# Kernel tuning notes

Measured on AMD Instinct MI355X. Metric: run time of the kernel, lower is better.

The kernel has to match this reference:

```python
import jax, jax.numpy as jnp
import numpy as np

B, S, D, H = 2, 2048, 2048, 16
HD = D // H
DFF = 4 * D
EPS = 1e-5


def _gelu(x):
    # tanh-approximate GELU as in the torch module
    c = jnp.sqrt(jnp.asarray(2.0 / jnp.pi, dtype=x.dtype))
    return 0.5 * x * (1.0 + jnp.tanh(c * (x + 0.044715 * x ** 3)))


def _layernorm(x, scale, shift):
    mean = jnp.mean(x, axis=-1, keepdims=True)
    var = jnp.mean((x - mean) ** 2, axis=-1, keepdims=True)  # unbiased=False
    return scale * (x - mean) / jnp.sqrt(var + EPS) + shift


def setup_inputs() -> dict:
    key = jax.random.key(0)
    ks = jax.random.split(key, 8)
    std = 0.02
    return {
        "x": jax.random.normal(ks[0], (B, S, D), dtype=jnp.float32),
        "Wq": std * jax.random.normal(ks[1], (D, D), dtype=jnp.float32),
        "Wk": std * jax.random.normal(ks[2], (D, D), dtype=jnp.float32),
        "Wv": std * jax.random.normal(ks[3], (D, D), dtype=jnp.float32),
        "Wo": std * jax.random.normal(ks[4], (D, D), dtype=jnp.float32),
        "bo": jnp.zeros((D,), dtype=jnp.float32),
        "ln1_scale": jnp.ones((D,), dtype=jnp.float32),
        "ln1_shift": jnp.zeros((D,), dtype=jnp.float32),
        "ln2_scale": jnp.ones((D,), dtype=jnp.float32),
        "ln2_shift": jnp.zeros((D,), dtype=jnp.float32),
        "W1": std * jax.random.normal(ks[5], (D, DFF), dtype=jnp.float32),
        "b1": jnp.zeros((DFF,), dtype=jnp.float32),
        "W2": std * jax.random.normal(ks[6], (DFF, D), dtype=jnp.float32),
        "b2": jnp.zeros((D,), dtype=jnp.float32),
    }


def _attention(x, Wq, Wk, Wv, Wo, bo):
    b, s, d = x.shape
    q = (x @ Wq).reshape(b, s, H, HD).transpose(0, 2, 1, 3)  # bhsd
    k = (x @ Wk).reshape(b, s, H, HD).transpose(0, 2, 1, 3)
    v = (x @ Wv).reshape(b, s, H, HD).transpose(0, 2, 1, 3)
    scores = jnp.einsum("bhqd,bhkd->bhqk", q, k)
    causal = jnp.tril(jnp.ones((s, s), dtype=bool))
    scores = jnp.where(causal, scores, -jnp.inf)
    w = jax.nn.softmax(scores / jnp.sqrt(jnp.asarray(HD, dtype=x.dtype)), axis=-1)
    ctx = jnp.einsum("bhqk,bhkd->bhqd", w, v)
    ctx = ctx.transpose(0, 2, 1, 3).reshape(b, s, d)
    return ctx @ Wo + bo


def reference(x, Wq, Wk, Wv, Wo, bo, ln1_scale, ln1_shift, ln2_scale, ln2_shift, W1, b1, W2, b2):
    # pre-LN transformer block; dropout rate 0 -> identity
    h = x + _attention(_layernorm(x, ln1_scale, ln1_shift), Wq, Wk, Wv, Wo, bo)
    y = _gelu(_layernorm(h, ln2_scale, ln2_shift) @ W1 + b1)
    return h + (y @ W2 + b2)
```

## Files before the change

kernel.cpp:

```cpp
#include <hip/hip_runtime.h>
#include <cmath>


typedef unsigned short u16;
typedef unsigned int   u32;
typedef float  f32x4  __attribute__((ext_vector_type(4)));
typedef short  s16x8  __attribute__((ext_vector_type(8)));
typedef short  s16x4  __attribute__((ext_vector_type(4)));
typedef __bf16 bf16x8 __attribute__((ext_vector_type(8)));

#define DEV __device__ __forceinline__

DEV u16 f2bf(float f) {
  union { float f; u32 u; } v; v.f = f;
  u32 u = v.u;
  u += 0x7fffu + ((u >> 16) & 1u);
  return (u16)(u >> 16);
}

DEV f32x4 mfma16(s16x8 a, s16x8 b, f32x4 c) {
  return __builtin_amdgcn_mfma_f32_16x16x32_bf16(
      __builtin_bit_cast(bf16x8, a), __builtin_bit_cast(bf16x8, b), c, 0, 0, 0);
}

DEV float gelu_f(float x) {
  const float c = 0.7978845608028654f;
  const float z = c * (x + 0.044715f * x * x * x);
  const float e = __expf(2.0f * z);
  const float th = 1.0f - 2.0f / (e + 1.0f);
  return 0.5f * x * (1.0f + th);
}

DEV void gload16(const u16* g, u16* l) {
  __builtin_amdgcn_global_load_lds(
      (const __attribute__((address_space(1))) u32*)(const void*)g,
      (__attribute__((address_space(3))) u32*)(void*)l, 16, 0, 0);
}

__global__ __launch_bounds__(256) void transpose_cast(
    const float* __restrict__ W, u16* __restrict__ Wt, int K, int N) {
  __shared__ float tile[32][33];
  const int n0 = blockIdx.x * 32, k0 = blockIdx.y * 32;
  const int tx = threadIdx.x, ty = threadIdx.y;
#pragma unroll
  for (int i = 0; i < 4; ++i)
    tile[ty + 8 * i][tx] = W[(size_t)(k0 + ty + 8 * i) * N + n0 + tx];
  __syncthreads();
#pragma unroll
  for (int i = 0; i < 4; ++i)
    Wt[(size_t)(n0 + ty + 8 * i) * K + k0 + tx] = f2bf(tile[tx][ty + 8 * i]);
}

__global__ __launch_bounds__(256) void transpose_v(
    const u16* __restrict__ QKV, u16* __restrict__ VT) {
  __shared__ u16 tile[32][33];
  const int s0 = blockIdx.x * 32;
  const int d0 = blockIdx.y * 32;
  const int bh = blockIdx.z;
  const int b = bh >> 4, h = bh & 15;
  const int tx = threadIdx.x, ty = threadIdx.y;
  const u16* src = QKV + (long)b * 2048 * 6144 + 4096 + h * 128;
#pragma unroll
  for (int i = 0; i < 4; ++i)
    tile[ty + 8 * i][tx] = src[(long)(s0 + ty + 8 * i) * 6144 + d0 + tx];
  __syncthreads();
  u16* dst = VT + (long)bh * 128 * 2048;
#pragma unroll
  for (int i = 0; i < 4; ++i)
    dst[(long)(d0 + ty + 8 * i) * 2048 + s0 + tx] = tile[tx][ty + 8 * i];
}

__global__ __launch_bounds__(256) void ln_kernel(
    const float* __restrict__ X, const float* __restrict__ sc,
    const float* __restrict__ sh, u16* __restrict__ Y) {
  const int row = blockIdx.x, t = threadIdx.x;
  const float* xr = X + (size_t)row * 2048;
  float4 v0 = ((const float4*)xr)[t];
  float4 v1 = ((const float4*)xr)[t + 256];
  float s  = v0.x + v0.y + v0.z + v0.w + v1.x + v1.y + v1.z + v1.w;
  float qs = v0.x*v0.x + v0.y*v0.y + v0.z*v0.z + v0.w*v0.w
           + v1.x*v1.x + v1.y*v1.y + v1.z*v1.z + v1.w*v1.w;
#pragma unroll
  for (int off = 1; off < 64; off <<= 1) {
    s  += __shfl_xor(s, off);
    qs += __shfl_xor(qs, off);
  }
  __shared__ float rs[4], rq[4];
  if ((t & 63) == 0) { rs[t >> 6] = s; rq[t >> 6] = qs; }
  __syncthreads();
  const float st = rs[0] + rs[1] + rs[2] + rs[3];
  const float qt = rq[0] + rq[1] + rq[2] + rq[3];
  const float mean = st * (1.0f / 2048.0f);
  const float var  = qt * (1.0f / 2048.0f) - mean * mean;
  const float rstd = rsqrtf(var + 1e-5f);

  u16* yr = Y + (size_t)row * 2048;
  const int c0 = t * 4, c1 = 1024 + t * 4;
  s16x4 o0, o1;
  o0[0] = (short)f2bf(sc[c0+0] * (v0.x - mean) * rstd + sh[c0+0]);
  o0[1] = (short)f2bf(sc[c0+1] * (v0.y - mean) * rstd + sh[c0+1]);
  o0[2] = (short)f2bf(sc[c0+2] * (v0.z - mean) * rstd + sh[c0+2]);
  o0[3] = (short)f2bf(sc[c0+3] * (v0.w - mean) * rstd + sh[c0+3]);
  o1[0] = (short)f2bf(sc[c1+0] * (v1.x - mean) * rstd + sh[c1+0]);
  o1[1] = (short)f2bf(sc[c1+1] * (v1.y - mean) * rstd + sh[c1+1]);
  o1[2] = (short)f2bf(sc[c1+2] * (v1.z - mean) * rstd + sh[c1+2]);
  o1[3] = (short)f2bf(sc[c1+3] * (v1.w - mean) * rstd + sh[c1+3]);
  *(s16x4*)(yr + c0) = o0;
  *(s16x4*)(yr + c1) = o1;
}

template<int MHALF, int STORE_BF16, int BIAS, int RES, int GELU_ACT>
__global__ __launch_bounds__(512, 2) void gemm8(
    const u16* __restrict__ A, const u16* __restrict__ Bt,
    const float* __restrict__ bias, const float* __restrict__ res,
    float* __restrict__ Cf, u16* __restrict__ Cb,
    int M, int N, int K, int rr, int rc) {
  constexpr int NPH   = 2 * MHALF;
  constexpr int ABUFS = (MHALF == 2) ? 2 : 3;
  constexpr int ASZ   = 8192 * MHALF;
  constexpr int BOFF  = ABUFS * ASZ;
  __shared__ u16 lds[BOFF + 2 * 16384];

  const int t9 = threadIdx.x;
  const int l = t9 & 63, w = t9 >> 6;
  const int r16 = l & 15, quad = l >> 4;
  const int wm = w >> 2, wn = w & 3;

  const int nbx = N >> 8;
  const int bid = blockIdx.x;
  const int xcd = bid & 7, j = bid >> 3;
  const int nregc = nbx / rc;
  const int m_t = (xcd / nregc) * rr + (j % rr);
  const int n_t = (xcd % nregc) * rc + (j / rr);
  const long m0 = (long)m_t * (128 * MHALF);
  const long n0 = (long)n_t * 256;

  const int NT = K >> 6;
  const int srow = t9 >> 3;
  const int scol = (t9 & 7) ^ (srow & 7);

  const u16* Abase = A  + (m0 + srow) * (long)K + scol * 8;
  const u16* Bbase = Bt + (n0 + srow) * (long)K + scol * 8;
  const long rowK64  = 64 * (long)K;
  const long rowK128 = 128 * (long)K;

  #define STAGE_A(tile, h) { \
    u16* d = &lds[((tile) % ABUFS) * ASZ + (h) * 8192 + w * 512]; \
    const u16* s = Abase + (h) * rowK128 + (long)(tile) * 64; \
    gload16(s, d); gload16(s + rowK64, d + 4096); }
  #define STAGE_B(tile, h) { \
    u16* d = &lds[BOFF + ((tile) & 1) * 16384 + (h) * 8192 + w * 512]; \
    const u16* s = Bbase + (h) * rowK128 + (long)(tile) * 64; \
    gload16(s, d); gload16(s + rowK64, d + 4096); }

  f32x4 acc[4 * MHALF][4] = {};

  if (MHALF == 2) {
    STAGE_B(0, 0); STAGE_B(0, 1); STAGE_A(0, 0); STAGE_A(0, 1);
    STAGE_B(1, 0); STAGE_B(1, 1);
    asm volatile("s_waitcnt vmcnt(4)" ::: "memory");
  } else {
    STAGE_B(0, 0); STAGE_B(0, 1); STAGE_A(0, 0); STAGE_A(1, 0);
    STAGE_B(1, 0); STAGE_B(1, 1);
    asm volatile("s_waitcnt vmcnt(6)" ::: "memory");
  }
  __builtin_amdgcn_sched_barrier(0);
  __builtin_amdgcn_s_barrier();

  s16x8 bf_[4][2];
  for (int t = 0; t < NT; ++t) {
    const int ab = t % ABUFS;
    const u16* Abuf = &lds[ab * ASZ];
    const u16* Bbuf = &lds[BOFF + (t & 1) * 16384];
#pragma unroll
    for (int p = 0; p < NPH; ++p) {
      if (p == 0) {
#pragma unroll
        for (int ni = 0; ni < 4; ++ni) {
          const int brow = wn * 64 + ni * 16 + r16;
#pragma unroll
          for (int ks = 0; ks < 2; ++ks)
            bf_[ni][ks] = *(const s16x8*)&Bbuf[brow * 64 + ((ks * 4 + quad) ^ (brow & 7)) * 8];
        }
      }
      s16x8 af[2][2];
#pragma unroll
      for (int mi = 0; mi < 2; ++mi) {
        const int arow = (MHALF == 2 ? wm * 128 : wm * 64) + (2 * p + mi) * 16 + r16;
#pragma unroll
        for (int ks = 0; ks < 2; ++ks)
          af[mi][ks] = *(const s16x8*)&Abuf[arow * 64 + ((ks * 4 + quad) ^ (arow & 7)) * 8];
      }
      if (MHALF == 2) {
        if (p < 2)       { if (t + 1 < NT) STAGE_A(t + 1, p); }
        else             { if (t + 2 < NT) STAGE_B(t + 2, p - 2); }
      } else {
        if (p == 0)      { if (t + 2 < NT) STAGE_A(t + 2, 0); }
        else             { if (t + 2 < NT) { STAGE_B(t + 2, 0); STAGE_B(t + 2, 1); } }
      }
      __builtin_amdgcn_sched_barrier(0);
      __builtin_amdgcn_s_barrier();
      asm volatile("s_waitcnt lgkmcnt(0)" ::: "memory");
      __builtin_amdgcn_sched_barrier(0);
      __builtin_amdgcn_s_setprio(1);
#pragma unroll
      for (int mi = 0; mi < 2; ++mi)
#pragma unroll
        for (int ni = 0; ni < 4; ++ni)
#pragma unroll
          for (int ks = 0; ks < 2; ++ks)
            acc[2 * p + mi][ni] = mfma16(af[mi][ks], bf_[ni][ks], acc[2 * p + mi][ni]);
      __builtin_amdgcn_s_setprio(0);
      __builtin_amdgcn_sched_barrier(0);
      if (p == NPH - 1) {
        if (MHALF == 2) {
          if (t + 2 < NT) { asm volatile("s_waitcnt vmcnt(4)" ::: "memory"); }
          else            { asm volatile("s_waitcnt vmcnt(0)" ::: "memory"); }
        } else {
          if (t + 2 < NT) { asm volatile("s_waitcnt vmcnt(6)" ::: "memory"); }
          else            { asm volatile("s_waitcnt vmcnt(0)" ::: "memory"); }
        }
        __builtin_amdgcn_sched_barrier(0);
      }
      __builtin_amdgcn_s_barrier();
    }
  }
  #undef STAGE_A
  #undef STAGE_B

#pragma unroll
  for (int mi = 0; mi < 4 * MHALF; ++mi) {
#pragma unroll
    for (int ni = 0; ni < 4; ++ni) {
#pragma unroll
      for (int r = 0; r < 4; ++r) {
        const long gr = m0 + (MHALF == 2 ? wm * 128 : wm * 64) + mi * 16 + quad * 4 + r;
        const long gc = n0 + wn * 64 + ni * 16 + r16;
        float v = acc[mi][ni][r];
        if (BIAS)     v += bias[gc];
        if (GELU_ACT) v  = gelu_f(v);
        if (RES)      v += res[gr * N + gc];
        if (STORE_BF16) Cb[gr * N + gc] = f2bf(v);
        else            Cf[gr * N + gc] = v;
      }
    }
  }
}

__global__ __launch_bounds__(256) void attn_kernel(
    const u16* __restrict__ QKV, const u16* __restrict__ VT,
    u16* __restrict__ CTX) {
  __shared__ u16 Ks[2][64 * 128];
  __shared__ u16 Vs[2][128 * 64];
  __shared__ u16 Pl[4][16 * 64];

  const int t = threadIdx.x;
  const int lane = t & 63, w = t >> 6;
  const int r16 = lane & 15, quad = lane >> 4;
  const int h = blockIdx.y, b = blockIdx.z;
  const long LDQ = 6144;
  const u16* Qb = QKV + (long)b * 2048 * LDQ + h * 128;
  const u16* Kb = Qb + 2048;
  const u16* Vtb = VT + (long)(b * 16 + h) * 128 * 2048;
  u16* Pw = Pl[w];
  const float scale = 0.08838834764831845f;

  const int k_row = t >> 4;
  const int k_slot = t & 15;
  const int v_row = t >> 3;
  const int v_slot = t & 7;

#define STAGE_KV(kt_, buf_)                                                    \
  {                                                                            \
    const int kb_ = (kt_) * 64;                                                \
    _Pragma("unroll") for (int i = 0; i < 4; ++i) {                            \
      const int row = i * 16 + k_row;                                          \
      gload16(Kb + (long)(kb_ + row) * LDQ + (k_slot ^ (row & 7)) * 8,         \
              &Ks[buf_][i * 2048 + w * 512]);                                  \
    }                                                                          \
    _Pragma("unroll") for (int i = 0; i < 4; ++i) {                            \
      const int d_ = i * 32 + v_row;                                           \
      gload16(Vtb + (long)d_ * 2048 + kb_ + (v_slot ^ (d_ & 7)) * 8,           \
              &Vs[buf_][i * 2048 + w * 512]);                                  \
    }                                                                          \
  }

  for (int half = 0; half < 2; ++half) {
    const int qt = half ? (31 - (int)blockIdx.x) : (int)blockIdx.x;
    const int qw = qt * 64 + w * 16;

    s16x8 aq[4];
#pragma unroll
    for (int ks = 0; ks < 4; ++ks)
      aq[ks] = *(const s16x8*)(Qb + (long)(qw + r16) * LDQ + ks * 32 + quad * 8);

    f32x4 o[8] = {};
    float mrun[4], lrun[4];
#pragma unroll
    for (int r = 0; r < 4; ++r) { mrun[r] = -1e30f; lrun[r] = 0.0f; }

    __builtin_amdgcn_s_barrier();
    STAGE_KV(0, 0);
    asm volatile("s_waitcnt vmcnt(0)" ::: "memory");
    __builtin_amdgcn_s_barrier();

    for (int kt = 0; kt <= qt; ++kt) {
      const int kbase = kt * 64;
      const int cur = kt & 1;
      if (kt < qt) STAGE_KV(kt + 1, cur ^ 1);

      if (kbase <= qw + 15) {
        f32x4 sc[4];
#pragma unroll
        for (int kh = 0; kh < 4; ++kh) {
          f32x4 z = {};
          sc[kh] = z;
          const int krow = kh * 16 + r16;
#pragma unroll
          for (int ks = 0; ks < 4; ++ks) {
            const s16x8 bk =
                *(const s16x8*)&Ks[cur][krow * 128 + ((ks * 4 + quad) ^ (krow & 7)) * 8];
            sc[kh] = mfma16(aq[ks], bk, sc[kh]);
          }
        }
        const bool need_mask = (kbase + 63 > qw);
        float alpha[4];
#pragma unroll
        for (int r = 0; r < 4; ++r) {
          const int q = qw + quad * 4 + r;
          float sv[4];
#pragma unroll
          for (int kh = 0; kh < 4; ++kh) {
            float s = sc[kh][r] * scale;
            if (need_mask && (kbase + kh * 16 + r16 > q)) s = -1e30f;
            sv[kh] = s;
          }
          float mx = fmaxf(fmaxf(sv[0], sv[1]), fmaxf(sv[2], sv[3]));
#pragma unroll
          for (int off = 1; off < 16; off <<= 1) mx = fmaxf(mx, __shfl_xor(mx, off));
          const float mn = fmaxf(mrun[r], mx);
          alpha[r] = __expf(mrun[r] - mn);
          mrun[r] = mn;
          const int prow = quad * 4 + r;
          float ps = 0.0f;
#pragma unroll
          for (int kh = 0; kh < 4; ++kh) {
            const float p = __expf(sv[kh] - mn);
            ps += p;
            Pw[(prow * 64 + kh * 16 + r16) ^ ((prow & 7) << 3)] = f2bf(p);
          }
          lrun[r] = lrun[r] * alpha[r] + ps;
        }
        if (alpha[0] != 1.0f || alpha[1] != 1.0f || alpha[2] != 1.0f || alpha[3] != 1.0f) {
#pragma unroll
          for (int ds = 0; ds < 8; ++ds)
#pragma unroll
            for (int r = 0; r < 4; ++r) o[ds][r] *= alpha[r];
        }
#pragma unroll
        for (int s = 0; s < 2; ++s) {
          const s16x8 ap =
              *(const s16x8*)&Pw[(r16 * 64 + s * 32 + quad * 8) ^ ((r16 & 7) << 3)];
#pragma unroll
          for (int ds = 0; ds < 8; ++ds) {
            const int d = ds * 16 + r16;
            const s16x8 bv =
                *(const s16x8*)&Vs[cur][d * 64 + ((s * 4 + quad) ^ (d & 7)) * 8];
            o[ds] = mfma16(ap, bv, o[ds]);
          }
        }
      }

      asm volatile("s_waitcnt vmcnt(0)" ::: "memory");
      __builtin_amdgcn_s_barrier();
    }

#pragma unroll
    for (int r = 0; r < 4; ++r)
#pragma unroll
      for (int off = 1; off < 16; off <<= 1) lrun[r] += __shfl_xor(lrun[r], off);

#pragma unroll
    for (int ds = 0; ds < 8; ++ds)
#pragma unroll
      for (int r = 0; r < 4; ++r) {
        const float v = o[ds][r] / lrun[r];
        CTX[(long)(b * 2048 + qw + quad * 4 + r) * 2048 + h * 128 + ds * 16 + r16] = f2bf(v);
      }
  }
#undef STAGE_KV
}

extern "C" void kernel_launch(void* const* d_in, const int* in_sizes, int n_in,
                              void* d_out, int out_size, void* d_ws, size_t ws_size,
                              hipStream_t stream) {
  (void)in_sizes; (void)n_in; (void)out_size; (void)ws_size;
  const float* x    = (const float*)d_in[0];
  const float* Wq   = (const float*)d_in[1];
  const float* Wk   = (const float*)d_in[2];
  const float* Wv   = (const float*)d_in[3];
  const float* Wo   = (const float*)d_in[4];
  const float* bo   = (const float*)d_in[5];
  const float* ln1s = (const float*)d_in[6];
  const float* ln1b = (const float*)d_in[7];
  const float* ln2s = (const float*)d_in[8];
  const float* ln2b = (const float*)d_in[9];
  const float* W1   = (const float*)d_in[10];
  const float* b1   = (const float*)d_in[11];
  const float* W2   = (const float*)d_in[12];
  const float* b2   = (const float*)d_in[13];
  float* out = (float*)d_out;

  const int Mtok = 4096, D = 2048, DFF = 8192, NQKV = 6144;

  char* w = (char*)d_ws;
  u16* Wt_qkv = (u16*)w;  w += (size_t)NQKV * D * 2;
  u16* Wt_o   = (u16*)w;  w += (size_t)D * D * 2;
  u16* Wt_1   = (u16*)w;  w += (size_t)DFF * D * 2;
  u16* Wt_2   = (u16*)w;  w += (size_t)D * DFF * 2;
  u16* Xln    = (u16*)w;  w += (size_t)Mtok * D * 2;
  u16* QKV    = (u16*)w;  w += (size_t)Mtok * NQKV * 2;
  u16* CTX    = (u16*)w;  w += (size_t)Mtok * D * 2;
  u16* Y1     = QKV;
  u16* VTb    = Wt_qkv;
  float* Hbuf = (float*)w; w += (size_t)Mtok * D * 4;

  const dim3 tb(32, 8, 1);
  transpose_cast<<<dim3(D / 32, D / 32), tb, 0, stream>>>(Wq, Wt_qkv,                    D, D);
  transpose_cast<<<dim3(D / 32, D / 32), tb, 0, stream>>>(Wk, Wt_qkv + (size_t)D * D,    D, D);
  transpose_cast<<<dim3(D / 32, D / 32), tb, 0, stream>>>(Wv, Wt_qkv + (size_t)2 * D * D,D, D);
  transpose_cast<<<dim3(D / 32, D / 32), tb, 0, stream>>>(Wo, Wt_o,                      D, D);
  transpose_cast<<<dim3(DFF / 32, D / 32), tb, 0, stream>>>(W1, Wt_1,                    D, DFF);
  transpose_cast<<<dim3(D / 32, DFF / 32), tb, 0, stream>>>(W2, Wt_2,                    DFF, D);

  ln_kernel<<<Mtok, 256, 0, stream>>>(x, ln1s, ln1b, Xln);

  gemm8<1, 1, 0, 0, 0><<<dim3(768), 512, 0, stream>>>(
      Xln, Wt_qkv, nullptr, nullptr, nullptr, QKV, Mtok, NQKV, D, 16, 6);

  transpose_v<<<dim3(64, 4, 32), tb, 0, stream>>>(QKV, VTb);

  attn_kernel<<<dim3(16, 16, 2), 256, 0, stream>>>(QKV, VTb, CTX);

  gemm8<1, 0, 1, 1, 0><<<dim3(256), 512, 0, stream>>>(
      CTX, Wt_o, bo, x, Hbuf, nullptr, Mtok, D, D, 8, 4);

  ln_kernel<<<Mtok, 256, 0, stream>>>(Hbuf, ln2s, ln2b, Xln);

  gemm8<2, 1, 1, 0, 1><<<dim3(512), 512, 0, stream>>>(
      Xln, Wt_1, b1, nullptr, nullptr, Y1, Mtok, DFF, D, 8, 8);

  gemm8<1, 0, 1, 1, 0><<<dim3(256), 512, 0, stream>>>(
      Y1, Wt_2, b2, Hbuf, out, nullptr, Mtok, D, DFF, 8, 4);
}
```

Before: 624.9 us.

## Add 256x256-tile GEMM kernel with split-K for FFN down-projection

Adds a dedicated gemm256 kernel with 256x256 output tiles and double-buffered A/B staging (four-phase schedule), used for the FFN up-projection. The down-projection now runs split-K over two K halves with a 256x256 tile (256 blocks), writing partial sums into a scratch buffer aliased onto the W1 weight workspace, followed by a separate reduce kernel that adds bias and residual. gemm8 is simplified to the 128-row path only. This is meant to raise data reuse and occupancy for the large GEMMs, at the cost of extra fp32 partial-sum traffic and an extra kernel launch.

```diff
diff --git a/kernel.cpp b/kernel.cpp
--- a/kernel.cpp
+++ b/kernel.cpp
@@ -4,10 +4,10 @@
 
 typedef unsigned short u16;
 typedef unsigned int   u32;
-typedef float  f32x4  __attribute__((ext_vector_type(4)));
-typedef short  s16x8  __attribute__((ext_vector_type(8)));
-typedef short  s16x4  __attribute__((ext_vector_type(4)));
-typedef __bf16 bf16x8 __attribute__((ext_vector_type(8)));
+typedef float  f32x4   __attribute__((ext_vector_type(4)));
+typedef short  s16x8   __attribute__((ext_vector_type(8)));
+typedef short  s16x4   __attribute__((ext_vector_type(4)));
+typedef __bf16 bf16x8  __attribute__((ext_vector_type(8)));
 
 #define DEV __device__ __forceinline__
 
@@ -109,15 +109,14 @@
   *(s16x4*)(yr + c1) = o1;
 }
 
-template<int MHALF, int STORE_BF16, int BIAS, int RES, int GELU_ACT>
+template<int STORE_BF16, int BIAS, int RES, int GELU_ACT>
 __global__ __launch_bounds__(512, 2) void gemm8(
     const u16* __restrict__ A, const u16* __restrict__ Bt,
     const float* __restrict__ bias, const float* __restrict__ res,
     float* __restrict__ Cf, u16* __restrict__ Cb,
     int M, int N, int K, int rr, int rc) {
-  constexpr int NPH   = 2 * MHALF;
-  constexpr int ABUFS = (MHALF == 2) ? 2 : 3;
-  constexpr int ASZ   = 8192 * MHALF;
+  constexpr int ABUFS = 3;
+  constexpr int ASZ   = 8192;
   constexpr int BOFF  = ABUFS * ASZ;
   __shared__ u16 lds[BOFF + 2 * 16384];
 
@@ -132,7 +131,7 @@
   const int nregc = nbx / rc;
   const int m_t = (xcd / nregc) * rr + (j % rr);
   const int n_t = (xcd % nregc) * rc + (j / rr);
-  const long m0 = (long)m_t * (128 * MHALF);
+  const long m0 = (long)m_t * 128;
   const long n0 = (long)n_t * 256;
 
   const int NT = K >> 6;
@@ -144,36 +143,29 @@
   const long rowK64  = 64 * (long)K;
   const long rowK128 = 128 * (long)K;
 
-  #define STAGE_A(tile, h) { \
+  #define STAGE_A8(tile, h) { \
     u16* d = &lds[((tile) % ABUFS) * ASZ + (h) * 8192 + w * 512]; \
     const u16* s = Abase + (h) * rowK128 + (long)(tile) * 64; \
     gload16(s, d); gload16(s + rowK64, d + 4096); }
-  #define STAGE_B(tile, h) { \
+  #define STAGE_B8(tile, h) { \
     u16* d = &lds[BOFF + ((tile) & 1) * 16384 + (h) * 8192 + w * 512]; \
     const u16* s = Bbase + (h) * rowK128 + (long)(tile) * 64; \
     gload16(s, d); gload16(s + rowK64, d + 4096); }
 
-  f32x4 acc[4 * MHALF][4] = {};
-
-  if (MHALF == 2) {
-    STAGE_B(0, 0); STAGE_B(0, 1); STAGE_A(0, 0); STAGE_A(0, 1);
-    STAGE_B(1, 0); STAGE_B(1, 1);
-    asm volatile("s_waitcnt vmcnt(4)" ::: "memory");
-  } else {
-    STAGE_B(0, 0); STAGE_B(0, 1); STAGE_A(0, 0); STAGE_A(1, 0);
-    STAGE_B(1, 0); STAGE_B(1, 1);
-    asm volatile("s_waitcnt vmcnt(6)" ::: "memory");
-  }
+  f32x4 acc[4][4] = {};
+
+  STAGE_B8(0, 0); STAGE_B8(0, 1); STAGE_A8(0, 0); STAGE_A8(1, 0);
+  STAGE_B8(1, 0); STAGE_B8(1, 1);
+  asm volatile("s_waitcnt vmcnt(6)" ::: "memory");
   __builtin_amdgcn_sched_barrier(0);
   __builtin_amdgcn_s_barrier();
 
   s16x8 bf_[4][2];
   for (int t = 0; t < NT; ++t) {
-    const int ab = t % ABUFS;
-    const u16* Abuf = &lds[ab * ASZ];
+    const u16* Abuf = &lds[(t % ABUFS) * ASZ];
     const u16* Bbuf = &lds[BOFF + (t & 1) * 16384];
 #pragma unroll
-    for (int p = 0; p < NPH; ++p) {
+    for (int p = 0; p < 2; ++p) {
       if (p == 0) {
 #pragma unroll
         for (int ni = 0; ni < 4; ++ni) {
@@ -186,18 +178,13 @@
       s16x8 af[2][2];
 #pragma unroll
       for (int mi = 0; mi < 2; ++mi) {
-        const int arow = (MHALF == 2 ? wm * 128 : wm * 64) + (2 * p + mi) * 16 + r16;
+        const int arow = wm * 64 + (2 * p + mi) * 16 + r16;
 #pragma unroll
         for (int ks = 0; ks < 2; ++ks)
           af[mi][ks] = *(const s16x8*)&Abuf[arow * 64 + ((ks * 4 + quad) ^ (arow & 7)) * 8];
       }
-      if (MHALF == 2) {
-        if (p < 2)       { if (t + 1 < NT) STAGE_A(t + 1, p); }
-        else             { if (t + 2 < NT) STAGE_B(t + 2, p - 2); }
-      } else {
-        if (p == 0)      { if (t + 2 < NT) STAGE_A(t + 2, 0); }
-        else             { if (t + 2 < NT) { STAGE_B(t + 2, 0); STAGE_B(t + 2, 1); } }
-      }
+      if (p == 0) { if (t + 2 < NT) STAGE_A8(t + 2, 0); }
+      else        { if (t + 2 < NT) { STAGE_B8(t + 2, 0); STAGE_B8(t + 2, 1); } }
       __builtin_amdgcn_sched_barrier(0);
       __builtin_amdgcn_s_barrier();
       asm volatile("s_waitcnt lgkmcnt(0)" ::: "memory");
@@ -212,29 +199,24 @@
             acc[2 * p + mi][ni] = mfma16(af[mi][ks], bf_[ni][ks], acc[2 * p + mi][ni]);
       __builtin_amdgcn_s_setprio(0);
       __builtin_amdgcn_sched_barrier(0);
-      if (p == NPH - 1) {
-        if (MHALF == 2) {
-          if (t + 2 < NT) { asm volatile("s_waitcnt vmcnt(4)" ::: "memory"); }
-          else            { asm volatile("s_waitcnt vmcnt(0)" ::: "memory"); }
-        } else {
-          if (t + 2 < NT) { asm volatile("s_waitcnt vmcnt(6)" ::: "memory"); }
-          else            { asm volatile("s_waitcnt vmcnt(0)" ::: "memory"); }
-        }
+      if (p == 1) {
+        if (t + 2 < NT) { asm volatile("s_waitcnt vmcnt(6)" ::: "memory"); }
+        else            { asm volatile("s_waitcnt vmcnt(0)" ::: "memory"); }
         __builtin_amdgcn_sched_barrier(0);
       }
       __builtin_amdgcn_s_barrier();
     }
   }
-  #undef STAGE_A
-  #undef STAGE_B
-
-#pragma unroll
-  for (int mi = 0; mi < 4 * MHALF; ++mi) {
+  #undef STAGE_A8
+  #undef STAGE_B8
+
+#pragma unroll
+  for (int mi = 0; mi < 4; ++mi) {
 #pragma unroll
     for (int ni = 0; ni < 4; ++ni) {
 #pragma unroll
       for (int r = 0; r < 4; ++r) {
-        const long gr = m0 + (MHALF == 2 ? wm * 128 : wm * 64) + mi * 16 + quad * 4 + r;
+        const long gr = m0 + wm * 64 + mi * 16 + quad * 4 + r;
         const long gc = n0 + wn * 64 + ni * 16 + r16;
         float v = acc[mi][ni][r];
         if (BIAS)     v += bias[gc];
@@ -244,6 +226,153 @@
         else            Cf[gr * N + gc] = v;
       }
     }
+  }
+}
+
+template<int STORE_BF16, int BIAS, int RES, int GELU_ACT, int SPLITK>
+__global__ __launch_bounds__(512, 2) void gemm256(
+    const u16* __restrict__ A, const u16* __restrict__ Bt,
+    const float* __restrict__ bias, const float* __restrict__ res,
+    float* __restrict__ Cf, u16* __restrict__ Cb, float* __restrict__ Cf2,
+    int M, int N, int K, int rr, int rc) {
+  __shared__ u16 ldsA[2 * 16384];
+  __shared__ u16 ldsB[2 * 16384];
+
+  const int t9 = threadIdx.x;
+  const int l = t9 & 63, w = t9 >> 6;
+  const int r16 = l & 15, quad = l >> 4;
+  const int wm = w >> 2, wn = w & 3;
+
+  const int nbx = N >> 8;
+  const int bid = blockIdx.x;
+  const int xcd = bid & 7, j = bid >> 3;
+  const int j2 = SPLITK ? (j >> 1) : j;
+  const int kh = SPLITK ? (j & 1) : 0;
+  const int nregc = nbx / rc;
+  const int m_t = (xcd / nregc) * rr + (j2 % rr);
+  const int n_t = (xcd % nregc) * rc + (j2 / rr);
+  const long m0 = (long)m_t * 256;
+  const long n0 = (long)n_t * 256;
+
+  const int Klen = SPLITK ? (K >> 1) : K;
+  const long koff = (long)kh * Klen;
+  const int NT = Klen >> 6;
+
+  const int srow = t9 >> 3;
+  const int scol = (t9 & 7) ^ (srow & 7);
+
+  const u16* Abase = A  + (m0 + srow) * (long)K + koff + scol * 8;
+  const u16* Bbase = Bt + (n0 + srow) * (long)K + koff + scol * 8;
+  const long rowK64 = 64 * (long)K;
+
+  #define STAGE_A2(tile, q) { \
+    u16* d = &ldsA[((tile) & 1) * 16384 + (q) * 4096 + w * 512]; \
+    gload16(Abase + (q) * rowK64 + (long)(tile) * 64, d); }
+  #define STAGE_B2(tile, q) { \
+    u16* d = &ldsB[((tile) & 1) * 16384 + (q) * 4096 + w * 512]; \
+    gload16(Bbase + (q) * rowK64 + (long)(tile) * 64, d); }
+
+  f32x4 acc[8][4] = {};
+
+  STAGE_B2(0, 0); STAGE_B2(0, 1); STAGE_B2(0, 2); STAGE_B2(0, 3);
+  STAGE_A2(0, 0); STAGE_A2(0, 2); STAGE_A2(0, 1); STAGE_A2(0, 3);
+  asm volatile("s_waitcnt vmcnt(2)" ::: "memory");
+  __builtin_amdgcn_sched_barrier(0);
+  __builtin_amdgcn_s_barrier();
+
+  s16x8 bf_[4][2];
+  for (int t = 0; t < NT; ++t) {
+    const u16* Abuf = &ldsA[(t & 1) * 16384];
+    const u16* Bbuf = &ldsB[(t & 1) * 16384];
+    const bool pre = (t + 1 < NT);
+#pragma unroll
+    for (int p = 0; p < 4; ++p) {
+      if (p == 0) {
+#pragma unroll
+        for (int ni = 0; ni < 4; ++ni) {
+          const int brow = wn * 64 + ni * 16 + r16;
+#pragma unroll
+          for (int ks = 0; ks < 2; ++ks)
+            bf_[ni][ks] = *(const s16x8*)&Bbuf[brow * 64 + ((ks * 4 + quad) ^ (brow & 7)) * 8];
+        }
+      }
+      s16x8 af[2][2];
+#pragma unroll
+      for (int mi = 0; mi < 2; ++mi) {
+        const int arow = wm * 128 + (2 * p + mi) * 16 + r16;
+#pragma unroll
+        for (int ks = 0; ks < 2; ++ks)
+          af[mi][ks] = *(const s16x8*)&Abuf[arow * 64 + ((ks * 4 + quad) ^ (arow & 7)) * 8];
+      }
+      if (pre) {
+        if (p == 0)      { STAGE_B2(t + 1, 0); STAGE_B2(t + 1, 1); }
+        else if (p == 1) { STAGE_B2(t + 1, 2); STAGE_B2(t + 1, 3); }
+        else if (p == 2) { STAGE_A2(t + 1, 0); STAGE_A2(t + 1, 2); }
+        else             { STAGE_A2(t + 1, 1); STAGE_A2(t + 1, 3); }
+      }
+      __builtin_amdgcn_sched_barrier(0);
+      __builtin_amdgcn_s_barrier();
+      asm volatile("s_waitcnt lgkmcnt(0)" ::: "memory");
+      __builtin_amdgcn_sched_barrier(0);
+      __builtin_amdgcn_s_setprio(1);
+#pragma unroll
+      for (int mi = 0; mi < 2; ++mi)
+#pragma unroll
+        for (int ni = 0; ni < 4; ++ni)
+#pragma unroll
+          for (int ks = 0; ks < 2; ++ks)
+            acc[2 * p + mi][ni] = mfma16(af[mi][ks], bf_[ni][ks], acc[2 * p + mi][ni]);
+      __builtin_amdgcn_s_setprio(0);
+      __builtin_amdgcn_sched_barrier(0);
+      if (p == 1) {
+        if (pre) { asm volatile("s_waitcnt vmcnt(4)" ::: "memory"); }
+        else     { asm volatile("s_waitcnt vmcnt(0)" ::: "memory"); }
+        __builtin_amdgcn_sched_barrier(0);
+      } else if (p == 3) {
+        if (pre) { asm volatile("s_waitcnt vmcnt(2)" ::: "memory"); }
+        __builtin_amdgcn_sched_barrier(0);
+      }
+      __builtin_amdgcn_s_barrier();
+    }
+  }
+  #undef STAGE_A2
+  #undef STAGE_B2
+
+  float* dstf = (SPLITK && kh) ? Cf2 : Cf;
+#pragma unroll
+  for (int mi = 0; mi < 8; ++mi) {
+#pragma unroll
+    for (int ni = 0; ni < 4; ++ni) {
+#pragma unroll
+      for (int r = 0; r < 4; ++r) {
+        const long gr = m0 + wm * 128 + mi * 16 + quad * 4 + r;
+        const long gc = n0 + wn * 64 + ni * 16 + r16;
+        float v = acc[mi][ni][r];
+        if (BIAS)     v += bias[gc];
+        if (GELU_ACT) v  = gelu_f(v);
+        if (RES)      v += res[gr * N + gc];
+        if (STORE_BF16) Cb[gr * N + gc] = f2bf(v);
+        else            dstf[gr * N + gc] = v;
+      }
+    }
+  }
+}
+
+__global__ __launch_bounds__(256) void splitk_reduce(
+    const float* __restrict__ p1, const float* __restrict__ res,
+    const float* __restrict__ bias, float* __restrict__ out, int N, long nf4) {
+  const long stride = (long)gridDim.x * 256;
+  for (long i = blockIdx.x * 256 + threadIdx.x; i < nf4; i += stride) {
+    float4 a = ((const float4*)out)[i];
+    float4 b = ((const float4*)p1)[i];
+    float4 r = ((const float4*)res)[i];
+    const int col = (int)((i * 4) % N);
+    float4 bb = *(const float4*)&bias[col];
+    a.x += b.x + r.x + bb.x;
+    a.y += b.y + r.y + bb.y;
+    a.z += b.z + r.z + bb.z;
+    a.w += b.w + r.w + bb.w;
+    ((float4*)out)[i] = a;
   }
 }
 
@@ -423,6 +552,7 @@
   u16* CTX    = (u16*)w;  w += (size_t)Mtok * D * 2;
   u16* Y1     = QKV;
   u16* VTb    = Wt_qkv;
+  float* P1   = (float*)Wt_1;
   float* Hbuf = (float*)w; w += (size_t)Mtok * D * 4;
 
   const dim3 tb(32, 8, 1);
@@ -435,21 +565,24 @@
 
   ln_kernel<<<Mtok, 256, 0, stream>>>(x, ln1s, ln1b, Xln);
 
-  gemm8<1, 1, 0, 0, 0><<<dim3(768), 512, 0, stream>>>(
+  gemm8<1, 0, 0, 0><<<dim3(768), 512, 0, stream>>>(
       Xln, Wt_qkv, nullptr, nullptr, nullptr, QKV, Mtok, NQKV, D, 16, 6);
 
   transpose_v<<<dim3(64, 4, 32), tb, 0, stream>>>(QKV, VTb);
 
   attn_kernel<<<dim3(16, 16, 2), 256, 0, stream>>>(QKV, VTb, CTX);
 
-  gemm8<1, 0, 1, 1, 0><<<dim3(256), 512, 0, stream>>>(
+  gemm8<0, 1, 1, 0><<<dim3(256), 512, 0, stream>>>(
       CTX, Wt_o, bo, x, Hbuf, nullptr, Mtok, D, D, 8, 4);
 
   ln_kernel<<<Mtok, 256, 0, stream>>>(Hbuf, ln2s, ln2b, Xln);
 
-  gemm8<2, 1, 1, 0, 1><<<dim3(512), 512, 0, stream>>>(
-      Xln, Wt_1, b1, nullptr, nullptr, Y1, Mtok, DFF, D, 8, 8);
-
-  gemm8<1, 0, 1, 1, 0><<<dim3(256), 512, 0, stream>>>(
-      Y1, Wt_2, b2, Hbuf, out, nullptr, Mtok, D, DFF, 8, 4);
-}
+  gemm256<1, 1, 0, 1, 0><<<dim3(512), 512, 0, stream>>>(
+      Xln, Wt_1, b1, nullptr, nullptr, Y1, nullptr, Mtok, DFF, D, 8, 8);
+
+  gemm256<0, 0, 0, 0, 1><<<dim3(256), 512, 0, stream>>>(
+      Y1, Wt_2, nullptr, nullptr, out, nullptr, P1, Mtok, D, DFF, 4, 4);
+
+  splitk_reduce<<<dim3(2048), 256, 0, stream>>>(
+      P1, Hbuf, b2, out, D, (long)Mtok * D / 4);
+}
```

Measured after the change: 687.2 us. 10.0% more time.
